# Performance work log

Hardware: AMD Instinct MI355X
Metric: run time of the kernel (lower is better)

Reference implementation:

```python
import jax, jax.numpy as jnp
import numpy as np

B, C_IN, C_OUT, E, H, W = 64, 384, 384, 8, 28, 28


def setup_inputs() -> dict:
    key = jax.random.key(0)
    k1, k2, k3 = jax.random.split(key, 3)
    x = jax.random.normal(k1, (B, C_IN, H, W), dtype=jnp.float32)
    routing_weights = jax.random.uniform(k2, (B, E), dtype=jnp.float32)
    # kaiming_normal_(mode='fan_out') per expert: std = sqrt(2 / fan_out), fan_out = out_channels * 1 * 1
    std = float(np.sqrt(2.0 / C_OUT))
    weight = jax.random.normal(k3, (E, C_OUT, C_IN), dtype=jnp.float32) * std
    return {"x": x, "routing_weights": routing_weights, "weight": weight}


def reference(x, routing_weights, weight):
    # Per-sample aggregated 1x1 conv weights: [b, c_out, c_in]
    agg = jnp.einsum('be,eoi->boi', routing_weights, weight)
    # Per-sample channel mixing (1x1 conv with groups=b == batched GEMM)
    out = jnp.einsum('boi,bihw->bohw', agg, x)
    return out
```

## Files before the change

### kernel.cpp

```cpp
#include <hip/hip_runtime.h>
#include <cstdint>

#define B_   64
#define CI_  384
#define CO_  384
#define HW_  784
#define E_   8

typedef unsigned short ushort_t;
typedef unsigned int   uint_t;

typedef __attribute__((ext_vector_type(8))) short bf16x8;
typedef __attribute__((ext_vector_type(4))) float f32x4;

__device__ __forceinline__ ushort_t f2bf_rne(float f) {
  uint_t u = __builtin_bit_cast(uint_t, f);
  u += 0x7fffu + ((u >> 16) & 1u);
  return (ushort_t)(u >> 16);
}

__device__ __forceinline__ uint_t pack_bf16_trunc(float f0, float f1) {
  return __builtin_amdgcn_perm(__builtin_bit_cast(uint_t, f1),
                               __builtin_bit_cast(uint_t, f0),
                               0x07060302u);
}

__global__ __launch_bounds__(256) void agg_kernel(const float* __restrict__ rw,
                                                  const float* __restrict__ w,
                                                  ushort_t* __restrict__ agg) {
  __shared__ float r[B_ * E_];
  const int tid = threadIdx.x;
  r[tid]       = rw[tid];
  r[tid + 256] = rw[tid + 256];
  const int base = blockIdx.x * 512 + tid * 2;
  float2 wv[E_];
#pragma unroll
  for (int e = 0; e < E_; ++e)
    wv[e] = *(const float2*)&w[e * (CO_ * CI_) + base];
  __syncthreads();
  const int b0 = blockIdx.y * 16;
#pragma unroll 4
  for (int bi = 0; bi < 16; ++bi) {
    const int b = b0 + bi;
    float ax = 0.f, ay = 0.f;
#pragma unroll
    for (int e = 0; e < E_; ++e) {
      const float rv = r[b * E_ + e];
      ax += rv * wv[e].x;
      ay += rv * wv[e].y;
    }
    const uint_t v = (uint_t)f2bf_rne(ax) | ((uint_t)f2bf_rne(ay) << 16);
    *(uint_t*)&agg[(size_t)b * (CO_ * CI_) + base] = v;
  }
}

#define BM 128
#define BN 128
#define BK 32
#define KIT (CI_ / BK)
#define BS_STRIDE 40

__global__ __launch_bounds__(256) void moe_gemm(const float* __restrict__ X,
                                                const ushort_t* __restrict__ Agg,
                                                float* __restrict__ Out) {
  __shared__ __align__(16) ushort_t As[BM * BK];
  __shared__ __align__(16) ushort_t Bs[BN * BS_STRIDE];

  const int tid  = threadIdx.x;
  const int lane = tid & 63;
  const int wave = tid >> 6;
  const int wm = wave & 1, wn = wave >> 1;

  const int bx = blockIdx.x;
  const int by = blockIdx.y;
  const int bg  = by / 21;
  const int rem = by - bg * 21;
  const int mt  = rem / 7;
  const int nt  = rem - mt * 7;
  const int b   = bg * 8 + bx;

  const ushort_t* Ab = Agg + (size_t)b * CO_ * CI_ + mt * BM * CI_;
  const float*    Xb = X   + (size_t)b * CI_ * HW_;

  const int sn  = tid & 127;
  const int sk4 = (tid >> 7) * 4;
  const int gn  = nt * BN + sn;
  const int gnc = gn < HW_ ? gn : (HW_ - 1);
  const float* Xcol = Xb + gnc;

  f32x4 acc[4][4];
#pragma unroll
  for (int i = 0; i < 4; ++i)
#pragma unroll
    for (int j = 0; j < 4; ++j)
      acc[i][j] = (f32x4)0.f;

  const int l15 = lane & 15;
  const int lq  = lane >> 4;
  const int xqA = lq ^ ((l15 >> 1) & 3);

  const int sm0 = tid >> 2,           sq0 = (tid & 3) ^ ((tid >> 3) & 3);
  const int sm1 = (tid + 256) >> 2,   sq1 = (tid & 3) ^ (((tid + 256) >> 3) & 3);

  for (int kk = 0; kk < KIT; ++kk) {
    const int k0 = kk * BK;
    {
      const ushort_t* src0 = Ab + sm0 * CI_ + k0 + sq0 * 8;
      __builtin_amdgcn_global_load_lds(
          (const __attribute__((address_space(1))) uint_t*)src0,
          (__attribute__((address_space(3))) uint_t*)&As[tid * 8], 16, 0, 0);
      const ushort_t* src1 = Ab + sm1 * CI_ + k0 + sq1 * 8;
      __builtin_amdgcn_global_load_lds(
          (const __attribute__((address_space(1))) uint_t*)src1,
          (__attribute__((address_space(3))) uint_t*)&As[(tid + 256) * 8], 16, 0, 0);
    }
#pragma unroll
    for (int j = 0; j < 4; ++j) {
      const int kl = j * 8 + sk4;
      const float* p = Xcol + (size_t)(k0 + kl) * HW_;
      const float v0 = p[0], v1 = p[HW_], v2 = p[2 * HW_], v3 = p[3 * HW_];
      const uint_t lo = pack_bf16_trunc(v0, v1);
      const uint_t hi = pack_bf16_trunc(v2, v3);
      *(uint2*)&Bs[sn * BS_STRIDE + kl] = make_uint2(lo, hi);
    }
    __syncthreads();
    bf16x8 a[4], bb[4];
#pragma unroll
    for (int mf = 0; mf < 4; ++mf) {
      const int m = wm * 64 + mf * 16 + l15;
      a[mf] = *(const bf16x8*)&As[(m * 4 + xqA) * 8];
    }
#pragma unroll
    for (int nf = 0; nf < 4; ++nf)
      bb[nf] = *(const bf16x8*)&Bs[(wn * 64 + nf * 16 + l15) * BS_STRIDE + lq * 8];
#pragma unroll
    for (int mf = 0; mf < 4; ++mf)
#pragma unroll
      for (int nf = 0; nf < 4; ++nf)
        acc[mf][nf] = __builtin_amdgcn_mfma_f32_16x16x32_bf16(a[mf], bb[nf],
                                                              acc[mf][nf], 0, 0, 0);
    __syncthreads();
  }

  float* Ob = Out + (size_t)b * CO_ * HW_;
#pragma unroll
  for (int mf = 0; mf < 4; ++mf) {
#pragma unroll
    for (int nf = 0; nf < 4; ++nf) {
      const int n = nt * BN + wn * 64 + nf * 16 + l15;
      if (n < HW_) {
        const int mbase = mt * BM + wm * 64 + mf * 16 + lq * 4;
#pragma unroll
        for (int r = 0; r < 4; ++r)
          Ob[(size_t)(mbase + r) * HW_ + n] = acc[mf][nf][r];
      }
    }
  }
}

extern "C" void kernel_launch(void* const* d_in, const int* in_sizes, int n_in,
                              void* d_out, int out_size, void* d_ws, size_t ws_size,
                              hipStream_t stream) {
  const float* x  = (const float*)d_in[0];
  const float* rw = (const float*)d_in[1];
  const float* w  = (const float*)d_in[2];
  float* out = (float*)d_out;
  ushort_t* agg = (ushort_t*)d_ws;

  agg_kernel<<<dim3((CO_ * CI_) / 512, 4), 256, 0, stream>>>(rw, w, agg);
  moe_gemm<<<dim3(8, 168), 256, 0, stream>>>(x, agg, out);
}
```

Before: 175.9 us.

## Double-buffer LDS tiles and overlap next-tile loads with MFMA compute

Splits the A and B shared-memory tiles into two buffers so the global loads for the next K tile are issued before the current tile's MFMAs, leaving one barrier per iteration instead of two. X is now loaded as float2 pairs covering 8 consecutive k rows per thread and written to LDS as 16-byte stores with an XOR-style offset to reduce bank conflicts. It also raises wave priority around the MFMA block and adds scheduling barriers to keep the loads ahead of the compute. This doubles LDS use and raises register pressure from the held X values, which may lower occupancy.

```diff
diff --git a/kernel.cpp b/kernel.cpp
--- a/kernel.cpp
+++ b/kernel.cpp
@@ -63,8 +63,8 @@
 __global__ __launch_bounds__(256) void moe_gemm(const float* __restrict__ X,
                                                 const ushort_t* __restrict__ Agg,
                                                 float* __restrict__ Out) {
-  __shared__ __align__(16) ushort_t As[BM * BK];
-  __shared__ __align__(16) ushort_t Bs[BN * BS_STRIDE];
+  __shared__ __align__(16) ushort_t As[2][BM * BK];
+  __shared__ __align__(16) ushort_t Bs[2][BN * BS_STRIDE];
 
   const int tid  = threadIdx.x;
   const int lane = tid & 63;
@@ -82,65 +82,106 @@
   const ushort_t* Ab = Agg + (size_t)b * CO_ * CI_ + mt * BM * CI_;
   const float*    Xb = X   + (size_t)b * CI_ * HW_;
 
-  const int sn  = tid & 127;
-  const int sk4 = (tid >> 7) * 4;
-  const int gn  = nt * BN + sn;
-  const int gnc = gn < HW_ ? gn : (HW_ - 1);
-  const float* Xcol = Xb + gnc;
-
-  f32x4 acc[4][4];
-#pragma unroll
-  for (int i = 0; i < 4; ++i)
-#pragma unroll
-    for (int j = 0; j < 4; ++j)
-      acc[i][j] = (f32x4)0.f;
+  const int nh  = tid & 63;
+  const int n0  = nh * 2;
+  const int kh  = (tid >> 6) * 8;
+  const int gn0 = nt * BN + n0;
+  const int gnc = gn0 > (HW_ - 2) ? (HW_ - 2) : gn0;
+  const float* Xcol = Xb + (size_t)kh * HW_ + gnc;
+
+  const int bwr0 = n0 * BS_STRIDE + kh + (((n0 >> 3) & 1) << 3);
+  const int bwr1 = (n0 + 1) * BS_STRIDE + kh + ((((n0 + 1) >> 3) & 1) << 3);
 
   const int l15 = lane & 15;
   const int lq  = lane >> 4;
   const int xqA = lq ^ ((l15 >> 1) & 3);
+  const int arow = ((wm * 64 + l15) * 4 + xqA) * 8;
+  const int brow = (wn * 64 + l15) * BS_STRIDE + lq * 8 + (((l15 >> 3) & 1) << 3);
 
   const int sm0 = tid >> 2,           sq0 = (tid & 3) ^ ((tid >> 3) & 3);
   const int sm1 = (tid + 256) >> 2,   sq1 = (tid & 3) ^ (((tid + 256) >> 3) & 3);
 
-  for (int kk = 0; kk < KIT; ++kk) {
-    const int k0 = kk * BK;
-    {
-      const ushort_t* src0 = Ab + sm0 * CI_ + k0 + sq0 * 8;
-      __builtin_amdgcn_global_load_lds(
-          (const __attribute__((address_space(1))) uint_t*)src0,
-          (__attribute__((address_space(3))) uint_t*)&As[tid * 8], 16, 0, 0);
-      const ushort_t* src1 = Ab + sm1 * CI_ + k0 + sq1 * 8;
-      __builtin_amdgcn_global_load_lds(
-          (const __attribute__((address_space(1))) uint_t*)src1,
-          (__attribute__((address_space(3))) uint_t*)&As[(tid + 256) * 8], 16, 0, 0);
-    }
-#pragma unroll
-    for (int j = 0; j < 4; ++j) {
-      const int kl = j * 8 + sk4;
-      const float* p = Xcol + (size_t)(k0 + kl) * HW_;
-      const float v0 = p[0], v1 = p[HW_], v2 = p[2 * HW_], v3 = p[3 * HW_];
-      const uint_t lo = pack_bf16_trunc(v0, v1);
-      const uint_t hi = pack_bf16_trunc(v2, v3);
-      *(uint2*)&Bs[sn * BS_STRIDE + kl] = make_uint2(lo, hi);
-    }
-    __syncthreads();
-    bf16x8 a[4], bb[4];
-#pragma unroll
-    for (int mf = 0; mf < 4; ++mf) {
-      const int m = wm * 64 + mf * 16 + l15;
-      a[mf] = *(const bf16x8*)&As[(m * 4 + xqA) * 8];
-    }
-#pragma unroll
-    for (int nf = 0; nf < 4; ++nf)
-      bb[nf] = *(const bf16x8*)&Bs[(wn * 64 + nf * 16 + l15) * BS_STRIDE + lq * 8];
-#pragma unroll
-    for (int mf = 0; mf < 4; ++mf)
-#pragma unroll
-      for (int nf = 0; nf < 4; ++nf)
-        acc[mf][nf] = __builtin_amdgcn_mfma_f32_16x16x32_bf16(a[mf], bb[nf],
-                                                              acc[mf][nf], 0, 0, 0);
-    __syncthreads();
-  }
+  f32x4 acc[4][4];
+#pragma unroll
+  for (int i = 0; i < 4; ++i)
+#pragma unroll
+    for (int j = 0; j < 4; ++j)
+      acc[i][j] = (f32x4)0.f;
+
+  float2 vr[8];
+
+#define STAGE_A(PB, K0)                                                        \
+  {                                                                            \
+    const ushort_t* s0_ = Ab + sm0 * CI_ + (K0) + sq0 * 8;                     \
+    __builtin_amdgcn_global_load_lds(                                          \
+        (const __attribute__((address_space(1))) uint_t*)s0_,                  \
+        (__attribute__((address_space(3))) uint_t*)&As[PB][tid * 8], 16, 0, 0);\
+    const ushort_t* s1_ = Ab + sm1 * CI_ + (K0) + sq1 * 8;                     \
+    __builtin_amdgcn_global_load_lds(                                          \
+        (const __attribute__((address_space(1))) uint_t*)s1_,                  \
+        (__attribute__((address_space(3))) uint_t*)&As[PB][(tid + 256) * 8],   \
+        16, 0, 0);                                                             \
+  }
+
+#define LOADB(K0)                                                              \
+  {                                                                            \
+    const float* p_ = Xcol + (size_t)(K0) * HW_;                               \
+    _Pragma("unroll") for (int k_ = 0; k_ < 8; ++k_)                           \
+        vr[k_] = *(const float2*)(p_ + (size_t)k_ * HW_);                      \
+  }
+
+#define PACKB(PB)                                                              \
+  {                                                                            \
+    const uint_t e0_ = pack_bf16_trunc(vr[0].x, vr[1].x);                      \
+    const uint_t e1_ = pack_bf16_trunc(vr[2].x, vr[3].x);                      \
+    const uint_t e2_ = pack_bf16_trunc(vr[4].x, vr[5].x);                      \
+    const uint_t e3_ = pack_bf16_trunc(vr[6].x, vr[7].x);                      \
+    *(uint4*)&Bs[PB][bwr0] = make_uint4(e0_, e1_, e2_, e3_);                   \
+    const uint_t o0_ = pack_bf16_trunc(vr[0].y, vr[1].y);                      \
+    const uint_t o1_ = pack_bf16_trunc(vr[2].y, vr[3].y);                      \
+    const uint_t o2_ = pack_bf16_trunc(vr[4].y, vr[5].y);                      \
+    const uint_t o3_ = pack_bf16_trunc(vr[6].y, vr[7].y);                      \
+    *(uint4*)&Bs[PB][bwr1] = make_uint4(o0_, o1_, o2_, o3_);                   \
+  }
+
+#define COMPUTE(CB)                                                            \
+  {                                                                            \
+    bf16x8 a_[4], b_[4];                                                       \
+    _Pragma("unroll") for (int mf_ = 0; mf_ < 4; ++mf_)                        \
+        a_[mf_] = *(const bf16x8*)&As[CB][arow + mf_ * (16 * BK)];             \
+    _Pragma("unroll") for (int nf_ = 0; nf_ < 4; ++nf_)                        \
+        b_[nf_] = *(const bf16x8*)&Bs[CB][brow + nf_ * (16 * BS_STRIDE)];      \
+    __builtin_amdgcn_s_setprio(1);                                             \
+    _Pragma("unroll") for (int mf_ = 0; mf_ < 4; ++mf_)                        \
+        _Pragma("unroll") for (int nf_ = 0; nf_ < 4; ++nf_)                    \
+            acc[mf_][nf_] = __builtin_amdgcn_mfma_f32_16x16x32_bf16(           \
+                a_[mf_], b_[nf_], acc[mf_][nf_], 0, 0, 0);                     \
+    __builtin_amdgcn_s_setprio(0);                                             \
+  }
+
+#define BODY(CB, PB, NT)                                                       \
+  {                                                                            \
+    STAGE_A(PB, (NT) * BK);                                                    \
+    LOADB((NT) * BK);                                                          \
+    __builtin_amdgcn_sched_barrier(0);                                         \
+    COMPUTE(CB);                                                               \
+    __builtin_amdgcn_sched_barrier(0);                                         \
+    PACKB(PB);                                                                 \
+    __syncthreads();                                                           \
+  }
+
+  STAGE_A(0, 0);
+  LOADB(0);
+  PACKB(0);
+  __syncthreads();
+
+#pragma unroll 1
+  for (int t = 0; t < 10; t += 2) {
+    BODY(0, 1, t + 1);
+    BODY(1, 0, t + 2);
+  }
+  BODY(0, 1, 11);
+  COMPUTE(1);
 
   float* Ob = Out + (size_t)b * CO_ * HW_;
 #pragma unroll
```

Result: slower. 181.5 us (+3.2%).

## Pre-convert X to bf16 k-packed layout and use LDS-free register GEMM

Applied to the files above, without the earlier changes.

A fused prep kernel now computes the aggregated weights and also converts X to bf16 in a layout that packs 8 channels per spatial position, written to workspace. The GEMM becomes a single-wave 48x112 tile kernel that loads MFMA fragments straight from global memory into registers, double-buffered, with no LDS and no barriers. The tile sizes divide 384 and 784 exactly, so the boundary checks are gone. The cost is an extra full pass writing and re-reading bf16 X, redundant global fragment loads across tiles, and heavy register use from 21 accumulators.

```diff
diff --git a/kernel.cpp b/kernel.cpp
--- a/kernel.cpp
+++ b/kernel.cpp
@@ -6,6 +6,7 @@
 #define CO_  384
 #define HW_  784
 #define E_   8
+#define G_   (CI_ / 8)
 
 typedef unsigned short ushort_t;
 typedef unsigned int   uint_t;
@@ -25,135 +26,139 @@
                                0x07060302u);
 }
 
-__global__ __launch_bounds__(256) void agg_kernel(const float* __restrict__ rw,
-                                                  const float* __restrict__ w,
-                                                  ushort_t* __restrict__ agg) {
+#define AGG_BLOCKS 1152
+#define XQ_BLOCKS  (G_ * B_)
+
+__global__ __launch_bounds__(256) void prep(const float* __restrict__ rw,
+                                            const float* __restrict__ w,
+                                            const float* __restrict__ x,
+                                            ushort_t* __restrict__ agg,
+                                            ushort_t* __restrict__ xq) {
   __shared__ float r[B_ * E_];
+  const int blk = blockIdx.x;
   const int tid = threadIdx.x;
-  r[tid]       = rw[tid];
-  r[tid + 256] = rw[tid + 256];
-  const int base = blockIdx.x * 512 + tid * 2;
-  float2 wv[E_];
+
+  if (blk < AGG_BLOCKS) {
+    r[tid]       = rw[tid];
+    r[tid + 256] = rw[tid + 256];
+    const int bxa = blk % 288;
+    const int bya = blk / 288;
+    const int base = bxa * 512 + tid * 2;
+    float2 wv[E_];
 #pragma unroll
-  for (int e = 0; e < E_; ++e)
-    wv[e] = *(const float2*)&w[e * (CO_ * CI_) + base];
-  __syncthreads();
-  const int b0 = blockIdx.y * 16;
+    for (int e = 0; e < E_; ++e)
+      wv[e] = *(const float2*)&w[e * (CO_ * CI_) + base];
+    __syncthreads();
+    const int b0 = bya * 16;
 #pragma unroll 4
-  for (int bi = 0; bi < 16; ++bi) {
-    const int b = b0 + bi;
-    float ax = 0.f, ay = 0.f;
+    for (int bi = 0; bi < 16; ++bi) {
+      const int b = b0 + bi;
+      float ax = 0.f, ay = 0.f;
 #pragma unroll
-    for (int e = 0; e < E_; ++e) {
-      const float rv = r[b * E_ + e];
-      ax += rv * wv[e].x;
-      ay += rv * wv[e].y;
+      for (int e = 0; e < E_; ++e) {
+        const float rv = r[b * E_ + e];
+        ax += rv * wv[e].x;
+        ay += rv * wv[e].y;
+      }
+      const uint_t v = (uint_t)f2bf_rne(ax) | ((uint_t)f2bf_rne(ay) << 16);
+      *(uint_t*)&agg[(size_t)b * (CO_ * CI_) + base] = v;
     }
-    const uint_t v = (uint_t)f2bf_rne(ax) | ((uint_t)f2bf_rne(ay) << 16);
-    *(uint_t*)&agg[(size_t)b * (CO_ * CI_) + base] = v;
+  } else {
+    const int idx = blk - AGG_BLOCKS;
+    const int g = idx % G_;
+    const int b = idx / G_;
+    const float* xp = x + ((size_t)b * CI_ + g * 8) * HW_;
+    ushort_t* op = xq + (((size_t)b * G_ + g) * HW_) * 8;
+#pragma unroll
+    for (int c = 0; c < 4; ++c) {
+      const int hw = c * 256 + tid;
+      if (hw < HW_) {
+        float v[8];
+#pragma unroll
+        for (int j = 0; j < 8; ++j) v[j] = xp[(size_t)j * HW_ + hw];
+        uint4 u;
+        u.x = pack_bf16_trunc(v[0], v[1]);
+        u.y = pack_bf16_trunc(v[2], v[3]);
+        u.z = pack_bf16_trunc(v[4], v[5]);
+        u.w = pack_bf16_trunc(v[6], v[7]);
+        *(uint4*)&op[hw * 8] = u;
+      }
+    }
   }
 }
 
-#define BM 128
-#define BN 128
-#define BK 32
-#define KIT (CI_ / BK)
-#define BS_STRIDE 40
+#define TM 48
+#define TN 112
+#define KIT 12
 
-__global__ __launch_bounds__(256) void moe_gemm(const float* __restrict__ X,
-                                                const ushort_t* __restrict__ Agg,
-                                                float* __restrict__ Out) {
-  __shared__ __align__(16) ushort_t As[BM * BK];
-  __shared__ __align__(16) ushort_t Bs[BN * BS_STRIDE];
-
-  const int tid  = threadIdx.x;
-  const int lane = tid & 63;
-  const int wave = tid >> 6;
-  const int wm = wave & 1, wn = wave >> 1;
+__global__ __launch_bounds__(64, 2) void moe_gemm2(const ushort_t* __restrict__ Agg,
+                                                   const ushort_t* __restrict__ Xq,
+                                                   float* __restrict__ Out) {
+  const int lane = threadIdx.x;
+  const int l15 = lane & 15;
+  const int lq  = lane >> 4;
 
   const int bx = blockIdx.x;
   const int by = blockIdx.y;
-  const int bg  = by / 21;
-  const int rem = by - bg * 21;
+  const int bg  = by / 56;
+  const int rem = by - bg * 56;
   const int mt  = rem / 7;
   const int nt  = rem - mt * 7;
   const int b   = bg * 8 + bx;
 
-  const ushort_t* Ab = Agg + (size_t)b * CO_ * CI_ + mt * BM * CI_;
-  const float*    Xb = X   + (size_t)b * CI_ * HW_;
+  const ushort_t* Abase = Agg + (size_t)b * CO_ * CI_ + (size_t)(mt * TM + l15) * CI_ + lq * 8;
+  const ushort_t* Bbase = Xq + (((size_t)b * G_ + lq) * HW_ + (nt * TN + l15)) * 8;
 
-  const int sn  = tid & 127;
-  const int sk4 = (tid >> 7) * 4;
-  const int gn  = nt * BN + sn;
-  const int gnc = gn < HW_ ? gn : (HW_ - 1);
-  const float* Xcol = Xb + gnc;
-
-  f32x4 acc[4][4];
+  f32x4 acc[3][7];
 #pragma unroll
-  for (int i = 0; i < 4; ++i)
+  for (int i = 0; i < 3; ++i)
 #pragma unroll
-    for (int j = 0; j < 4; ++j)
+    for (int j = 0; j < 7; ++j)
       acc[i][j] = (f32x4)0.f;
 
-  const int l15 = lane & 15;
-  const int lq  = lane >> 4;
-  const int xqA = lq ^ ((l15 >> 1) & 3);
+  bf16x8 a0[3], a1[3], b0v[7], b1v[7];
 
-  const int sm0 = tid >> 2,           sq0 = (tid & 3) ^ ((tid >> 3) & 3);
-  const int sm1 = (tid + 256) >> 2,   sq1 = (tid & 3) ^ (((tid + 256) >> 3) & 3);
+#define LA(dst, KK)                                                            \
+  {                                                                            \
+    _Pragma("unroll") for (int mf_ = 0; mf_ < 3; ++mf_)                        \
+        dst[mf_] = *(const bf16x8*)(Abase + (KK) * 32 + mf_ * (16 * CI_));     \
+  }
+#define LB(dst, KK)                                                            \
+  {                                                                            \
+    _Pragma("unroll") for (int nf_ = 0; nf_ < 7; ++nf_)                        \
+        dst[nf_] = *(const bf16x8*)(Bbase + (KK) * (4 * HW_ * 8) + nf_ * 128); \
+  }
+#define MM(A_, B_)                                                             \
+  {                                                                            \
+    _Pragma("unroll") for (int mf_ = 0; mf_ < 3; ++mf_)                        \
+        _Pragma("unroll") for (int nf_ = 0; nf_ < 7; ++nf_)                    \
+            acc[mf_][nf_] = __builtin_amdgcn_mfma_f32_16x16x32_bf16(           \
+                A_[mf_], B_[nf_], acc[mf_][nf_], 0, 0, 0);                     \
+  }
 
-  for (int kk = 0; kk < KIT; ++kk) {
-    const int k0 = kk * BK;
-    {
-      const ushort_t* src0 = Ab + sm0 * CI_ + k0 + sq0 * 8;
-      __builtin_amdgcn_global_load_lds(
-          (const __attribute__((address_space(1))) uint_t*)src0,
-          (__attribute__((address_space(3))) uint_t*)&As[tid * 8], 16, 0, 0);
-      const ushort_t* src1 = Ab + sm1 * CI_ + k0 + sq1 * 8;
-      __builtin_amdgcn_global_load_lds(
-          (const __attribute__((address_space(1))) uint_t*)src1,
-          (__attribute__((address_space(3))) uint_t*)&As[(tid + 256) * 8], 16, 0, 0);
-    }
-#pragma unroll
-    for (int j = 0; j < 4; ++j) {
-      const int kl = j * 8 + sk4;
-      const float* p = Xcol + (size_t)(k0 + kl) * HW_;
-      const float v0 = p[0], v1 = p[HW_], v2 = p[2 * HW_], v3 = p[3 * HW_];
-      const uint_t lo = pack_bf16_trunc(v0, v1);
-      const uint_t hi = pack_bf16_trunc(v2, v3);
-      *(uint2*)&Bs[sn * BS_STRIDE + kl] = make_uint2(lo, hi);
-    }
-    __syncthreads();
-    bf16x8 a[4], bb[4];
-#pragma unroll
-    for (int mf = 0; mf < 4; ++mf) {
-      const int m = wm * 64 + mf * 16 + l15;
-      a[mf] = *(const bf16x8*)&As[(m * 4 + xqA) * 8];
-    }
-#pragma unroll
-    for (int nf = 0; nf < 4; ++nf)
-      bb[nf] = *(const bf16x8*)&Bs[(wn * 64 + nf * 16 + l15) * BS_STRIDE + lq * 8];
-#pragma unroll
-    for (int mf = 0; mf < 4; ++mf)
-#pragma unroll
-      for (int nf = 0; nf < 4; ++nf)
-        acc[mf][nf] = __builtin_amdgcn_mfma_f32_16x16x32_bf16(a[mf], bb[nf],
-                                                              acc[mf][nf], 0, 0, 0);
-    __syncthreads();
+  LA(a0, 0); LB(b0v, 0);
+#pragma unroll 1
+  for (int t = 0; t < 5; ++t) {
+    const int k1 = 2 * t + 1, k2 = 2 * t + 2;
+    LA(a1, k1); LB(b1v, k1);
+    MM(a0, b0v);
+    LA(a0, k2); LB(b0v, k2);
+    MM(a1, b1v);
   }
+  LA(a1, 11); LB(b1v, 11);
+  MM(a0, b0v);
+  MM(a1, b1v);
 
   float* Ob = Out + (size_t)b * CO_ * HW_;
 #pragma unroll
-  for (int mf = 0; mf < 4; ++mf) {
+  for (int mf = 0; mf < 3; ++mf) {
 #pragma unroll
-    for (int nf = 0; nf < 4; ++nf) {
-      const int n = nt * BN + wn * 64 + nf * 16 + l15;
-      if (n < HW_) {
-        const int mbase = mt * BM + wm * 64 + mf * 16 + lq * 4;
+    for (int nf = 0; nf < 7; ++nf) {
+      const int n = nt * TN + nf * 16 + l15;
+      const int mbase = mt * TM + mf * 16 + lq * 4;
 #pragma unroll
-        for (int r = 0; r < 4; ++r)
-          Ob[(size_t)(mbase + r) * HW_ + n] = acc[mf][nf][r];
-      }
+      for (int r = 0; r < 4; ++r)
+        Ob[(size_t)(mbase + r) * HW_ + n] = acc[mf][nf][r];
     }
   }
 }
@@ -165,8 +170,10 @@
   const float* rw = (const float*)d_in[1];
   const float* w  = (const float*)d_in[2];
   float* out = (float*)d_out;
+
   ushort_t* agg = (ushort_t*)d_ws;
+  ushort_t* xq  = agg + (size_t)B_ * CO_ * CI_;
 
-  agg_kernel<<<dim3((CO_ * CI_) / 512, 4), 256, 0, stream>>>(rw, w, agg);
-  moe_gemm<<<dim3(8, 168), 256, 0, stream>>>(x, agg, out);
+  prep<<<AGG_BLOCKS + XQ_BLOCKS, 256, 0, stream>>>(rw, w, x, agg, xq);
+  moe_gemm2<<<dim3(8, 448), 64, 0, stream>>>(agg, xq, out);
 }
```

Result: no change. 178.2 us (+1.3%).
